# Performance work log

Hardware: AMD Instinct MI355X
Metric: run time of the kernel (lower is better)

## Reference

```python
import jax, jax.numpy as jnp
import numpy as np

N_NODES = 50000
N_EDGES = 800000
IN_FEATS = 128
N_HIDDEN = 64
OUT_FEATS = 40
DIM = 8  # pseudo-coordinate dimension
K = 1    # n_kernels


def setup_inputs() -> dict:
    key = jax.random.key(0)
    ks = jax.random.split(key, 12)
    inp = {
        "features": jax.random.normal(ks[0], (N_NODES, IN_FEATS), dtype=jnp.float32),
        "edge_weight": jax.random.normal(ks[1], (N_EDGES, DIM), dtype=jnp.float32),
        "src": jax.random.randint(ks[2], (N_EDGES,), 0, N_NODES),
        "dst": jax.random.randint(ks[3], (N_EDGES,), 0, N_NODES),
        # layer 1 params (fc has no bias in DGL GMMConv; separate additive bias)
        "W1": jax.random.normal(ks[4], (IN_FEATS, K * N_HIDDEN), dtype=jnp.float32) * (1.0 / np.sqrt(IN_FEATS)),
        "b1": jnp.zeros((N_HIDDEN,), dtype=jnp.float32),
        "mu1": jax.random.normal(ks[5], (K, DIM), dtype=jnp.float32) * 0.1,
        "inv_sigma1": jnp.ones((K, DIM), dtype=jnp.float32),
        # layer 2 params
        "W2": jax.random.normal(ks[6], (N_HIDDEN, K * OUT_FEATS), dtype=jnp.float32) * (1.0 / np.sqrt(N_HIDDEN)),
        "b2": jnp.zeros((OUT_FEATS,), dtype=jnp.float32),
        "mu2": jax.random.normal(ks[7], (K, DIM), dtype=jnp.float32) * 0.1,
        "inv_sigma2": jnp.ones((K, DIM), dtype=jnp.float32),
    }
    return inp


def gmm_conv(x, pseudo, src, dst, W, b, mu, inv_sigma, out_feats):
    # x: [N, in], pseudo: [E, DIM], W: [in, K*out]
    h = (x @ W).reshape(-1, K, out_feats)                      # [N, K, out]
    # gaussian mixture weights per edge/kernel: [E, K]
    diff = pseudo[:, None, :] - mu[None, :, :]                 # [E, K, DIM]
    gw = jnp.exp(-0.5 * jnp.sum(diff * diff * (inv_sigma[None] ** 2), axis=-1))
    # gather src feats, weight, sum over kernels: [E, out]
    msg = jnp.einsum("ekf,ek->ef", h[src], gw)
    agg = jax.ops.segment_sum(msg, dst, num_segments=N_NODES)  # [N, out]
    return agg + b


def reference(features, edge_weight, src, dst, W1, b1, mu1, inv_sigma1, W2, b2, mu2, inv_sigma2):
    x = gmm_conv(features, edge_weight, src, dst, W1, b1, mu1, inv_sigma1, N_HIDDEN)
    x = gmm_conv(x, edge_weight, src, dst, W2, b2, mu2, inv_sigma2, OUT_FEATS)
    return jax.nn.log_softmax(x, axis=1)
```

## Files before the change

kernel.cpp:

```cpp
#include <hip/hip_runtime.h>
#include <hip/hip_fp16.h>
#include <math.h>

#define N_NODES 50000
#define N_EDGES 800000
#define IN_FEATS 128
#define N_HIDDEN 64
#define OUT_FEATS 40
#define DIM 8
#define SCAN_NB ((N_NODES + 255) / 256)
#define GT_TILES ((N_NODES + 63) / 64)
#define FILL_NB 1024

typedef _Float16 half8 __attribute__((ext_vector_type(8)));
typedef float floatx4 __attribute__((ext_vector_type(4)));

__device__ __forceinline__ int wave_incl_scan(int x, int lane) {
#pragma unroll
    for (int off = 1; off < 64; off <<= 1) {
        int v = __shfl_up(x, off, 64);
        if (lane >= off) x += v;
    }
    return x;
}

__global__ __launch_bounds__(256) void hist_kernel(const int* __restrict__ dst,
                                                   int* __restrict__ counts) {
    int i = blockIdx.x * 256 + threadIdx.x;
    if (i * 4 >= N_EDGES) return;
    int4 d = ((const int4*)dst)[i];
    atomicAdd(&counts[d.x], 1);
    atomicAdd(&counts[d.y], 1);
    atomicAdd(&counts[d.z], 1);
    atomicAdd(&counts[d.w], 1);
}

__global__ __launch_bounds__(256) void scan_kernel(const int* __restrict__ counts,
                                                   int* __restrict__ offsets,
                                                   int* __restrict__ cursor,
                                                   int* __restrict__ partials) {
    const int tid = threadIdx.x, bid = blockIdx.x;
    int i = bid * 256 + tid;
    int lane = tid & 63, wid = tid >> 6;
    int x = (i < N_NODES) ? counts[i] : 0;
    int incl = wave_incl_scan(x, lane);
    __shared__ int wsum[4];
    __shared__ int sExc, sTot;
    if (lane == 63) wsum[wid] = incl;
    __syncthreads();
    int base = 0;
#pragma unroll
    for (int w = 0; w < 4; ++w)
        if (w < wid) base += wsum[w];
    int lexcl = base + incl - x;
    if (tid == 255) sTot = base + incl;
    __syncthreads();
    if (tid == 0) {
        int T = sTot;
        if (bid == 0) {
            __hip_atomic_store(&partials[0], (T << 2) | 2,
                               __ATOMIC_RELAXED, __HIP_MEMORY_SCOPE_AGENT);
            sExc = 0;
        } else {
            __hip_atomic_store(&partials[bid], (T << 2) | 1,
                               __ATOMIC_RELAXED, __HIP_MEMORY_SCOPE_AGENT);
            int sum = 0, pb = bid - 1;
            while (true) {
                int v = __hip_atomic_load(&partials[pb],
                                          __ATOMIC_RELAXED, __HIP_MEMORY_SCOPE_AGENT);
                if (v == 0) continue;
                sum += v >> 2;
                if ((v & 3) == 2) break;
                --pb;
            }
            __hip_atomic_store(&partials[bid], ((sum + T) << 2) | 2,
                               __ATOMIC_RELAXED, __HIP_MEMORY_SCOPE_AGENT);
            sExc = sum;
        }
    }
    __syncthreads();
    int E = sExc;
    if (i < N_NODES) {
        int v = E + lexcl;
        offsets[i] = v;
        cursor[i]  = v;
    }
    if (bid == SCAN_NB - 1 && tid == 0) offsets[N_NODES] = N_EDGES;
}

__global__ __launch_bounds__(256) void fillgemm_kernel(
    const float* __restrict__ features, const float* __restrict__ W1,
    const int* __restrict__ src, const int* __restrict__ dst,
    const float* __restrict__ ew,
    const float* __restrict__ mu1, const float* __restrict__ is1,
    const float* __restrict__ mu2, const float* __restrict__ is2,
    int* __restrict__ cursor, int2* __restrict__ csr,
    __half* __restrict__ h1)
{
    const int tid = threadIdx.x;
    __shared__ __align__(16) __half WT[64][136];

    if (blockIdx.x >= GT_TILES) {
        int fb = blockIdx.x - GT_TILES;
        for (int e = fb * 256 + tid; e < N_EDGES; e += FILL_NB * 256) {
            const float4* ew4 = (const float4*)(ew + (size_t)e * DIM);
            float4 wa = ew4[0], wb = ew4[1];
            float v[8] = {wa.x, wa.y, wa.z, wa.w, wb.x, wb.y, wb.z, wb.w};
            float s1 = 0.f, s2 = 0.f;
#pragma unroll
            for (int d = 0; d < DIM; ++d) {
                float d1 = v[d] - mu1[d]; float a1 = is1[d];
                float d2 = v[d] - mu2[d]; float a2 = is2[d];
                s1 += d1 * d1 * a1 * a1;
                s2 += d2 * d2 * a2 * a2;
            }
            __half2 g = __floats2half2_rn(expf(-0.5f * s1), expf(-0.5f * s2));
            int2 rec;
            rec.x = src[e];
            rec.y = *reinterpret_cast<int*>(&g);
            int pos = atomicAdd(&cursor[dst[e]], 1);
            csr[pos] = rec;
        }
        return;
    }

    int nodeBase = blockIdx.x * 64;
    for (int rep = 0; rep < 32; ++rep) {
        int idx = tid + rep * 256;
        int k = idx >> 6, n = idx & 63;
        WT[n][k] = __float2half(W1[idx]);
    }
    __syncthreads();

    int lane = tid & 63, w = tid >> 6;
    int m = lane & 15, quad = lane >> 4;
    int row = nodeBase + w * 16 + m;
    int rowc = (row < N_NODES) ? row : (N_NODES - 1);
    const float* fr = features + (size_t)rowc * IN_FEATS;

    floatx4 acc0 = {0.f,0.f,0.f,0.f}, acc1 = acc0, acc2 = acc0, acc3 = acc0;
#pragma unroll
    for (int kc = 0; kc < 4; ++kc) {
        float4 fa = *(const float4*)(fr + kc * 32 + quad * 8);
        float4 fb = *(const float4*)(fr + kc * 32 + quad * 8 + 4);
        union { half8 v; __half2 h2[4]; } A;
        A.h2[0] = __floats2half2_rn(fa.x, fa.y);
        A.h2[1] = __floats2half2_rn(fa.z, fa.w);
        A.h2[2] = __floats2half2_rn(fb.x, fb.y);
        A.h2[3] = __floats2half2_rn(fb.z, fb.w);
        half8 b0 = *(const half8*)&WT[ 0 + m][kc * 32 + quad * 8];
        half8 b1 = *(const half8*)&WT[16 + m][kc * 32 + quad * 8];
        half8 b2 = *(const half8*)&WT[32 + m][kc * 32 + quad * 8];
        half8 b3 = *(const half8*)&WT[48 + m][kc * 32 + quad * 8];
        acc0 = __builtin_amdgcn_mfma_f32_16x16x32_f16(A.v, b0, acc0, 0, 0, 0);
        acc1 = __builtin_amdgcn_mfma_f32_16x16x32_f16(A.v, b1, acc1, 0, 0, 0);
        acc2 = __builtin_amdgcn_mfma_f32_16x16x32_f16(A.v, b2, acc2, 0, 0, 0);
        acc3 = __builtin_amdgcn_mfma_f32_16x16x32_f16(A.v, b3, acc3, 0, 0, 0);
    }
    int nodeRow = nodeBase + w * 16 + quad * 4;
#pragma unroll
    for (int r = 0; r < 4; ++r) {
        int n = nodeRow + r;
        if (n < N_NODES) {
            size_t base = (size_t)n * N_HIDDEN + m;
            h1[base +  0] = __float2half(acc0[r]);
            h1[base + 16] = __float2half(acc1[r]);
            h1[base + 32] = __float2half(acc2[r]);
            h1[base + 48] = __float2half(acc3[r]);
        }
    }
}

__global__ __launch_bounds__(256) void agg1_gemm2_kernel(const __half* __restrict__ h,
                                                         const int* __restrict__ offsets,
                                                         const int2* __restrict__ csr,
                                                         const float* __restrict__ b,
                                                         const float* __restrict__ W2,
                                                         __half* __restrict__ h2) {
    __shared__ float xs[8][64];
    const unsigned* h32 = (const unsigned*)h;
    const int tid = threadIdx.x;
    const int w = tid >> 6, lane = tid & 63;
    const int hf = lane >> 5, p = lane & 31;
    const int ln = w * 2 + hf;
    const int n = blockIdx.x * 8 + ln;
    int beg = offsets[n], end = offsets[n + 1];

    float ax = 0.f, ay = 0.f;
    int j = beg;
    for (; j + 4 <= end; j += 4) {
        int2 r0 = csr[j + 0], r1 = csr[j + 1], r2 = csr[j + 2], r3 = csr[j + 3];
        unsigned v0 = h32[(size_t)r0.x * 32 + p];
        unsigned v1 = h32[(size_t)r1.x * 32 + p];
        unsigned v2 = h32[(size_t)r2.x * 32 + p];
        unsigned v3 = h32[(size_t)r3.x * 32 + p];
        float g0 = __low2float(*reinterpret_cast<__half2*>(&r0.y));
        float g1 = __low2float(*reinterpret_cast<__half2*>(&r1.y));
        float g2 = __low2float(*reinterpret_cast<__half2*>(&r2.y));
        float g3 = __low2float(*reinterpret_cast<__half2*>(&r3.y));
        float2 f0 = __half22float2(*reinterpret_cast<__half2*>(&v0));
        float2 f1 = __half22float2(*reinterpret_cast<__half2*>(&v1));
        float2 f2 = __half22float2(*reinterpret_cast<__half2*>(&v2));
        float2 f3 = __half22float2(*reinterpret_cast<__half2*>(&v3));
        ax += f0.x * g0; ay += f0.y * g0;
        ax += f1.x * g1; ay += f1.y * g1;
        ax += f2.x * g2; ay += f2.y * g2;
        ax += f3.x * g3; ay += f3.y * g3;
    }
    for (; j < end; ++j) {
        int2 r = csr[j];
        unsigned v = h32[(size_t)r.x * 32 + p];
        float g = __low2float(*reinterpret_cast<__half2*>(&r.y));
        float2 f = __half22float2(*reinterpret_cast<__half2*>(&v));
        ax += f.x * g; ay += f.y * g;
    }
    float2 bb = *(const float2*)&b[2 * p];
    *(float2*)&xs[ln][2 * p] = make_float2(ax + bb.x, ay + bb.y);
    __syncthreads();

    for (int o = tid; o < 8 * OUT_FEATS; o += 256) {
        int node = o / OUT_FEATS, t = o % OUT_FEATS;
        const float* xr = xs[node];
        float acc = 0.f;
#pragma unroll
        for (int k = 0; k < N_HIDDEN; ++k)
            acc += xr[k] * W2[k * OUT_FEATS + t];
        h2[(size_t)(blockIdx.x * 8 + node) * OUT_FEATS + t] = __float2half(acc);
    }
}

__global__ __launch_bounds__(256) void agg2_kernel(const __half* __restrict__ h,
                                                   const int* __restrict__ offsets,
                                                   const int2* __restrict__ csr,
                                                   const float* __restrict__ b,
                                                   float* __restrict__ out) {
    const unsigned* h32 = (const unsigned*)h;
    const int tid = threadIdx.x;
    const int w = tid >> 6, lane = tid & 63;
    const int hf = lane >> 5, p = lane & 31;
    const int n = blockIdx.x * 8 + w * 2 + hf;
    const int pc = (p < 20) ? p : 19;
    int beg = offsets[n], end = offsets[n + 1];

    float ax = 0.f, ay = 0.f;
    int j = beg;
    for (; j + 4 <= end; j += 4) {
        int2 r0 = csr[j + 0], r1 = csr[j + 1], r2 = csr[j + 2], r3 = csr[j + 3];
        unsigned v0 = h32[(size_t)r0.x * 20 + pc];
        unsigned v1 = h32[(size_t)r1.x * 20 + pc];
        unsigned v2 = h32[(size_t)r2.x * 20 + pc];
        unsigned v3 = h32[(size_t)r3.x * 20 + pc];
        float g0 = __high2float(*reinterpret_cast<__half2*>(&r0.y));
        float g1 = __high2float(*reinterpret_cast<__half2*>(&r1.y));
        float g2 = __high2float(*reinterpret_cast<__half2*>(&r2.y));
        float g3 = __high2float(*reinterpret_cast<__half2*>(&r3.y));
        float2 f0 = __half22float2(*reinterpret_cast<__half2*>(&v0));
        float2 f1 = __half22float2(*reinterpret_cast<__half2*>(&v1));
        float2 f2 = __half22float2(*reinterpret_cast<__half2*>(&v2));
        float2 f3 = __half22float2(*reinterpret_cast<__half2*>(&v3));
        ax += f0.x * g0; ay += f0.y * g0;
        ax += f1.x * g1; ay += f1.y * g1;
        ax += f2.x * g2; ay += f2.y * g2;
        ax += f3.x * g3; ay += f3.y * g3;
    }
    for (; j < end; ++j) {
        int2 r = csr[j];
        unsigned v = h32[(size_t)r.x * 20 + pc];
        float g = __high2float(*reinterpret_cast<__half2*>(&r.y));
        float2 f = __half22float2(*reinterpret_cast<__half2*>(&v));
        ax += f.x * g; ay += f.y * g;
    }

    bool valid = (p < 20);
    float vx = valid ? ax + b[2 * p]     : -INFINITY;
    float vy = valid ? ay + b[2 * p + 1] : -INFINITY;
    float m = fmaxf(vx, vy);
#pragma unroll
    for (int off = 16; off; off >>= 1)
        m = fmaxf(m, __shfl_xor(m, off, 32));
    float ex = valid ? (expf(vx - m) + expf(vy - m)) : 0.f;
#pragma unroll
    for (int off = 16; off; off >>= 1)
        ex += __shfl_xor(ex, off, 32);
    float ls = logf(ex);
    if (valid) {
        float2 o = make_float2(vx - m - ls, vy - m - ls);
        *(float2*)&out[(size_t)n * OUT_FEATS + 2 * p] = o;
    }
}

extern "C" void kernel_launch(void* const* d_in, const int* in_sizes, int n_in,
                              void* d_out, int out_size, void* d_ws, size_t ws_size,
                              hipStream_t stream) {
    const float* features    = (const float*)d_in[0];
    const float* edge_weight = (const float*)d_in[1];
    const int*   src         = (const int*)d_in[2];
    const int*   dst         = (const int*)d_in[3];
    const float* W1          = (const float*)d_in[4];
    const float* b1          = (const float*)d_in[5];
    const float* mu1         = (const float*)d_in[6];
    const float* is1         = (const float*)d_in[7];
    const float* W2          = (const float*)d_in[8];
    const float* b2          = (const float*)d_in[9];
    const float* mu2         = (const float*)d_in[10];
    const float* is2         = (const float*)d_in[11];
    float* out = (float*)d_out;

    int2*   csr     = (int2*)d_ws;
    __half* h1      = (__half*)(csr + N_EDGES);
    __half* h2      = h1 + (size_t)N_NODES * N_HIDDEN;
    int*    counts  = (int*)(h2 + (size_t)N_NODES * OUT_FEATS);
    int*    partials= counts + N_NODES;
    int*    cursor  = partials + 256;
    int*    offsets = cursor + N_NODES;

    hipMemsetAsync(counts, 0, (N_NODES + 256) * sizeof(int), stream);

    hist_kernel<<<(N_EDGES / 4 + 255) / 256, 256, 0, stream>>>(dst, counts);

    scan_kernel<<<SCAN_NB, 256, 0, stream>>>(counts, offsets, cursor, partials);

    fillgemm_kernel<<<GT_TILES + FILL_NB, 256, 0, stream>>>(
        features, W1, src, dst, edge_weight, mu1, is1, mu2, is2, cursor, csr, h1);

    agg1_gemm2_kernel<<<N_NODES / 8, 256, 0, stream>>>(h1, offsets, csr, b1, W2, h2);

    agg2_kernel<<<N_NODES / 8, 256, 0, stream>>>(h2, offsets, csr, b2, out);
}
```

Measured before the change: 261.1 us.

## Use single-block chunked scan and 4-edge-per-thread CSR fill

Replaces the multi-block decoupled-lookback prefix scan with a single 1024-thread block in which each thread scans a 52-element chunk loaded as int4. This removes the serial lookback chain and the partials memset. The CSR fill now gives each thread four consecutive edges with vectorized src/dst loads, issues its atomics early, and hoists the mu/sigma loads, instead of a grid-stride loop over 1024 blocks. The single-block scan runs on one CU, so its latency depends on that block's serial chunk work.

```diff
diff --git a/kernel.cpp b/kernel.cpp
--- a/kernel.cpp
+++ b/kernel.cpp
@@ -8,9 +8,9 @@
 #define N_HIDDEN 64
 #define OUT_FEATS 40
 #define DIM 8
-#define SCAN_NB ((N_NODES + 255) / 256)
 #define GT_TILES ((N_NODES + 63) / 64)
-#define FILL_NB 1024
+#define FILL_BLOCKS ((N_EDGES / 4 + 255) / 256)
+#define SCHUNK 52
 
 typedef _Float16 half8 __attribute__((ext_vector_type(8)));
 typedef float floatx4 __attribute__((ext_vector_type(4)));
@@ -35,57 +35,54 @@
     atomicAdd(&counts[d.w], 1);
 }
 
-__global__ __launch_bounds__(256) void scan_kernel(const int* __restrict__ counts,
-                                                   int* __restrict__ offsets,
-                                                   int* __restrict__ cursor,
-                                                   int* __restrict__ partials) {
-    const int tid = threadIdx.x, bid = blockIdx.x;
-    int i = bid * 256 + tid;
-    int lane = tid & 63, wid = tid >> 6;
-    int x = (i < N_NODES) ? counts[i] : 0;
-    int incl = wave_incl_scan(x, lane);
-    __shared__ int wsum[4];
-    __shared__ int sExc, sTot;
+__global__ __launch_bounds__(1024) void scan_kernel(const int* __restrict__ counts,
+                                                    int* __restrict__ offsets,
+                                                    int* __restrict__ cursor) {
+    const int tid = threadIdx.x;
+    const int lane = tid & 63, wid = tid >> 6;
+    const int beg = tid * SCHUNK;
+
+    int4 c[SCHUNK / 4];
+    int s = 0;
+#pragma unroll
+    for (int j = 0; j < SCHUNK / 4; ++j) {
+        int idx = beg + j * 4;
+        if (idx < N_NODES) {
+            c[j] = *(const int4*)(counts + idx);
+        } else {
+            c[j] = make_int4(0, 0, 0, 0);
+        }
+        s += c[j].x + c[j].y + c[j].z + c[j].w;
+    }
+
+    __shared__ int wsum[16];
+    int incl = wave_incl_scan(s, lane);
     if (lane == 63) wsum[wid] = incl;
     __syncthreads();
-    int base = 0;
-#pragma unroll
-    for (int w = 0; w < 4; ++w)
-        if (w < wid) base += wsum[w];
-    int lexcl = base + incl - x;
-    if (tid == 255) sTot = base + incl;
+    if (wid == 0) {
+        int v = (lane < 16) ? wsum[lane] : 0;
+        int sc = wave_incl_scan(v, lane);
+        if (lane < 16) wsum[lane] = sc;
+    }
     __syncthreads();
-    if (tid == 0) {
-        int T = sTot;
-        if (bid == 0) {
-            __hip_atomic_store(&partials[0], (T << 2) | 2,
-                               __ATOMIC_RELAXED, __HIP_MEMORY_SCOPE_AGENT);
-            sExc = 0;
-        } else {
-            __hip_atomic_store(&partials[bid], (T << 2) | 1,
-                               __ATOMIC_RELAXED, __HIP_MEMORY_SCOPE_AGENT);
-            int sum = 0, pb = bid - 1;
-            while (true) {
-                int v = __hip_atomic_load(&partials[pb],
-                                          __ATOMIC_RELAXED, __HIP_MEMORY_SCOPE_AGENT);
-                if (v == 0) continue;
-                sum += v >> 2;
-                if ((v & 3) == 2) break;
-                --pb;
-            }
-            __hip_atomic_store(&partials[bid], ((sum + T) << 2) | 2,
-                               __ATOMIC_RELAXED, __HIP_MEMORY_SCOPE_AGENT);
-            sExc = sum;
+    int wbase = (wid > 0) ? wsum[wid - 1] : 0;
+    int run = wbase + incl - s;
+
+#pragma unroll
+    for (int j = 0; j < SCHUNK / 4; ++j) {
+        int idx = beg + j * 4;
+        if (idx < N_NODES) {
+            int4 v = c[j];
+            int4 o;
+            o.x = run; run += v.x;
+            o.y = run; run += v.y;
+            o.z = run; run += v.z;
+            o.w = run; run += v.w;
+            *(int4*)(offsets + idx) = o;
+            *(int4*)(cursor  + idx) = o;
         }
     }
-    __syncthreads();
-    int E = sExc;
-    if (i < N_NODES) {
-        int v = E + lexcl;
-        offsets[i] = v;
-        cursor[i]  = v;
-    }
-    if (bid == SCAN_NB - 1 && tid == 0) offsets[N_NODES] = N_EDGES;
+    if (tid == 0) offsets[N_NODES] = N_EDGES;
 }
 
 __global__ __launch_bounds__(256) void fillgemm_kernel(
@@ -102,25 +99,51 @@
 
     if (blockIdx.x >= GT_TILES) {
         int fb = blockIdx.x - GT_TILES;
-        for (int e = fb * 256 + tid; e < N_EDGES; e += FILL_NB * 256) {
-            const float4* ew4 = (const float4*)(ew + (size_t)e * DIM);
-            float4 wa = ew4[0], wb = ew4[1];
+        int t = fb * 256 + tid;
+        if (t * 4 >= N_EDGES) return;
+
+        int4 s4 = ((const int4*)src)[t];
+        int4 d4 = ((const int4*)dst)[t];
+        int p0 = atomicAdd(&cursor[d4.x], 1);
+        int p1 = atomicAdd(&cursor[d4.y], 1);
+        int p2 = atomicAdd(&cursor[d4.z], 1);
+        int p3 = atomicAdd(&cursor[d4.w], 1);
+
+        const float4* ew4 = (const float4*)(ew + (size_t)t * 4 * DIM);
+        float4 wa0 = ew4[0], wb0 = ew4[1];
+        float4 wa1 = ew4[2], wb1 = ew4[3];
+        float4 wa2 = ew4[4], wb2 = ew4[5];
+        float4 wa3 = ew4[6], wb3 = ew4[7];
+
+        float M1[8], Q1[8], M2[8], Q2[8];
+#pragma unroll
+        for (int d = 0; d < DIM; ++d) {
+            M1[d] = mu1[d]; float a1 = is1[d]; Q1[d] = a1 * a1;
+            M2[d] = mu2[d]; float a2 = is2[d]; Q2[d] = a2 * a2;
+        }
+
+        auto gauss = [&](const float4& wa, const float4& wb) -> int {
             float v[8] = {wa.x, wa.y, wa.z, wa.w, wb.x, wb.y, wb.z, wb.w};
             float s1 = 0.f, s2 = 0.f;
 #pragma unroll
             for (int d = 0; d < DIM; ++d) {
-                float d1 = v[d] - mu1[d]; float a1 = is1[d];
-                float d2 = v[d] - mu2[d]; float a2 = is2[d];
-                s1 += d1 * d1 * a1 * a1;
-                s2 += d2 * d2 * a2 * a2;
+                float d1 = v[d] - M1[d];
+                float d2 = v[d] - M2[d];
+                s1 += d1 * d1 * Q1[d];
+                s2 += d2 * d2 * Q2[d];
             }
             __half2 g = __floats2half2_rn(expf(-0.5f * s1), expf(-0.5f * s2));
-            int2 rec;
-            rec.x = src[e];
-            rec.y = *reinterpret_cast<int*>(&g);
-            int pos = atomicAdd(&cursor[dst[e]], 1);
-            csr[pos] = rec;
-        }
+            return *reinterpret_cast<int*>(&g);
+        };
+
+        int2 r0 = make_int2(s4.x, gauss(wa0, wb0));
+        int2 r1 = make_int2(s4.y, gauss(wa1, wb1));
+        int2 r2 = make_int2(s4.z, gauss(wa2, wb2));
+        int2 r3 = make_int2(s4.w, gauss(wa3, wb3));
+        csr[p0] = r0;
+        csr[p1] = r1;
+        csr[p2] = r2;
+        csr[p3] = r3;
         return;
     }
 
@@ -313,14 +336,15 @@
     int*    partials= counts + N_NODES;
     int*    cursor  = partials + 256;
     int*    offsets = cursor + N_NODES;
-
-    hipMemsetAsync(counts, 0, (N_NODES + 256) * sizeof(int), stream);
+    (void)partials;
+
+    hipMemsetAsync(counts, 0, N_NODES * sizeof(int), stream);
 
     hist_kernel<<<(N_EDGES / 4 + 255) / 256, 256, 0, stream>>>(dst, counts);
 
-    scan_kernel<<<SCAN_NB, 256, 0, stream>>>(counts, offsets, cursor, partials);
-
-    fillgemm_kernel<<<GT_TILES + FILL_NB, 256, 0, stream>>>(
+    scan_kernel<<<1, 1024, 0, stream>>>(counts, offsets, cursor);
+
+    fillgemm_kernel<<<GT_TILES + FILL_BLOCKS, 256, 0, stream>>>(
         features, W1, src, dst, edge_weight, mu1, is1, mu2, is2, cursor, csr, h1);
 
     agg1_gemm2_kernel<<<N_NODES / 8, 256, 0, stream>>>(h1, offsets, csr, b1, W2, h2);
```

After: 269.7 us. 1.03x slower.
